# Kernel tuning notes

Hardware: AMD Instinct MI355X
Metric: run time of the kernel (lower is better)

The kernel has to match this reference:

```python
import jax, jax.numpy as jnp
import numpy as np

B, N, E, D, OUT, L = 4, 10000, 160000, 128, 64, 4
NEG = 0.01  # LeakyReLU slope

def lrelu(x):
    return jnp.where(x > 0, x, NEG * x)

def setup_inputs() -> dict:
    key = jax.random.key(0)
    ks = jax.random.split(key, 20)
    s = 0.05
    inp = {
        "x": jax.random.normal(ks[0], (B, N * 3), dtype=jnp.float32),
        "edge_index": jax.random.randint(ks[1], (2, E), 0, N, dtype=jnp.int32),
        # f0: Linear(3, D)
        "w0": jax.random.normal(ks[2], (3, D), dtype=jnp.float32) * s,
        "b0": jax.random.normal(ks[3], (D,), dtype=jnp.float32) * s,
        # per-layer params stacked on leading L axis
        "ew1": jax.random.normal(ks[4], (L, 2 * D + 1, D), dtype=jnp.float32) * s,
        "eb1": jax.random.normal(ks[5], (L, D), dtype=jnp.float32) * s,
        "ew2": jax.random.normal(ks[6], (L, D, D), dtype=jnp.float32) * s,
        "eb2": jax.random.normal(ks[7], (L, D), dtype=jnp.float32) * s,
        "cw": jax.random.normal(ks[8], (L, D, 1), dtype=jnp.float32) * s,
        "cb": jax.random.normal(ks[9], (L, 1), dtype=jnp.float32) * s,
        "nw1": jax.random.normal(ks[10], (L, 2 * D, D), dtype=jnp.float32) * s,
        "nb1": jax.random.normal(ks[11], (L, D), dtype=jnp.float32) * s,
        "nw2": jax.random.normal(ks[12], (L, D, D), dtype=jnp.float32) * s,
        "nb2": jax.random.normal(ks[13], (L, D), dtype=jnp.float32) * s,
        # project: Linear(D, OUT)
        "wp": jax.random.normal(ks[14], (D, OUT), dtype=jnp.float32) * s,
        "bp": jax.random.normal(ks[15], (OUT,), dtype=jnp.float32) * s,
    }
    return inp

def reference(x, edge_index, w0, b0, ew1, eb1, ew2, eb2, cw, cb, nw1, nb1, nw2, nb2, wp, bp):
    b = x.shape[0]
    n = x.shape[1] // 3
    pos = x.reshape(b, n, 3)            # coordinates [B,N,3]
    h = lrelu(pos @ w0 + b0)            # node features [B,N,D]
    row, col = edge_index[0], edge_index[1]
    # per-node in-edge counts (same for all layers/batches); scatter_mean -> 0 for empty nodes
    cnt = jnp.zeros((n,), x.dtype).at[col].add(1.0)
    denom = jnp.maximum(cnt, 1.0)[None, :, None]
    for i in range(L):
        rel = pos[:, row] - pos[:, col]                          # [B,E,3]
        dist_sq = jnp.sum(rel * rel, axis=-1, keepdims=True)     # [B,E,1]
        edge_in = jnp.concatenate([h[:, row], h[:, col], dist_sq], axis=-1)  # [B,E,2D+1]
        msg = lrelu(lrelu(edge_in @ ew1[i] + eb1[i]) @ ew2[i] + eb2[i])       # [B,E,D]
        aggr = jnp.zeros((b, n, msg.shape[-1]), msg.dtype).at[:, col].add(msg) / denom  # scatter_mean
        coord_update = jnp.tanh(aggr @ cw[i] + cb[i])            # [B,N,1]
        pos = pos + coord_update * 0.1
        node_in = jnp.concatenate([h, aggr], axis=-1)            # [B,N,2D]
        h = h + lrelu(lrelu(node_in @ nw1[i] + nb1[i]) @ nw2[i] + nb2[i])
    return lrelu(h.mean(axis=1) @ wp + bp)                       # [B,OUT]
```

## Files before the change

kernel.cpp:

```cpp
#include <hip/hip_runtime.h>
#include <hip/hip_bf16.h>
#include <math.h>

#define BB   4
#define NN   10000
#define NP   10112
#define EE   160000
#define DD   128
#define OUTD 64
#define LL   4
#define NEGS 0.01f
#define MSTR 136
#define RSF  34

typedef __attribute__((ext_vector_type(8))) short   short8;
typedef __attribute__((ext_vector_type(4))) float   floatx4;
typedef __attribute__((ext_vector_type(4))) uint    uintx4;

__device__ __forceinline__ float lrelu(float x) { return fmaxf(x, NEGS * x); }
__device__ __forceinline__ ushort f2bf(float x) {
    uint u = __builtin_bit_cast(uint, x);
    return (ushort)((u + 0x7FFFu + ((u >> 16) & 1u)) >> 16);
}
__device__ __forceinline__ float bf2f(ushort u) {
    uint v = ((uint)u) << 16;
    return __builtin_bit_cast(float, v);
}
__device__ __forceinline__ float bcf(uint u) { return __builtin_bit_cast(float, u); }

__global__ void k_cvtw_all(const float* __restrict__ ew1, const float* __restrict__ ew2,
                           const float* __restrict__ nw1, const float* __restrict__ nw2,
                           ushort* __restrict__ wtopf, ushort* __restrict__ wmidf,
                           ushort* __restrict__ ew2f, ushort* __restrict__ nw1f,
                           ushort* __restrict__ nw2f) {
    int tid = blockIdx.x * 256 + threadIdx.x;
    const float* src; ushort* dst; int pitch, nks, loc;
    if (tid < 8192)       { src = ew1;                     dst = wtopf; pitch = 257; nks = 4; loc = tid; }
    else if (tid < 16384) { src = ew1 + (size_t)128 * DD;  dst = wmidf; pitch = 257; nks = 4; loc = tid - 8192; }
    else if (tid < 24576) { src = ew2;                     dst = ew2f;  pitch = 128; nks = 4; loc = tid - 16384; }
    else if (tid < 40960) { src = nw1;                     dst = nw1f;  pitch = 256; nks = 8; loc = tid - 24576; }
    else                  { src = nw2;                     dst = nw2f;  pitch = 128; nks = 4; loc = tid - 40960; }
    int lane = loc & 63;
    int nt   = (loc >> 6) & 7;
    int ks   = (loc >> 9) % nks;
    int l    = loc / (nks * 512);
    int quad = lane >> 4, l16 = lane & 15;
    int n = nt * 16 + l16;
    const float* s = src + (size_t)l * pitch * DD;
    ushort* d = dst + (size_t)loc * 8;
    #pragma unroll
    for (int j = 0; j < 8; ++j)
        d[j] = f2bf(s[(size_t)(ks * 32 + quad * 8 + j) * DD + n]);
}

__global__ void k_h0(const float* __restrict__ x, const float* __restrict__ w0,
                     const float* __restrict__ b0, ushort* __restrict__ hb) {
    int idx = blockIdx.x * 256 + threadIdx.x;
    if (idx >= BB * NP * DD) return;
    int d  = idx & (DD - 1);
    int bn = idx >> 7;
    int n  = bn % NP, b = bn / NP;
    float v = 0.0f;
    if (n < NN) {
        const float* p = x + ((size_t)b * NN + n) * 3;
        v = lrelu(b0[d] + p[0] * w0[d] + p[1] * w0[DD + d] + p[2] * w0[2 * DD + d]);
    }
    hb[idx] = f2bf(v);
}

__global__ void k_count(const int* __restrict__ col, float* __restrict__ cnt,
                        int* __restrict__ ecnt) {
    int e = blockIdx.x * blockDim.x + threadIdx.x;
    if (e < EE) {
        int c = col[e];
        atomicAdd(&cnt[c], 1.0f);
        atomicAdd(&ecnt[c], 1);
    }
}

__global__ __launch_bounds__(256) void k_scan(const int* __restrict__ ecnt,
                                              int* __restrict__ cursor) {
    __shared__ int s_sum[256];
    int t = threadIdx.x;
    int base = t * 40;
    int s = 0;
    for (int i = 0; i < 40; ++i) {
        int n = base + i;
        if (n < NN) s += ecnt[n];
    }
    s_sum[t] = s;
    __syncthreads();
    if (t == 0) {
        int a = 0;
        for (int i = 0; i < 256; ++i) { int v = s_sum[i]; s_sum[i] = a; a += v; }
    }
    __syncthreads();
    int a = s_sum[t];
    for (int i = 0; i < 40; ++i) {
        int n = base + i;
        if (n < NN) { cursor[n] = a; a += ecnt[n]; }
    }
}

__global__ void k_place(const int* __restrict__ row, const int* __restrict__ col,
                        int* __restrict__ cursor,
                        int* __restrict__ rowS, int* __restrict__ colS) {
    int e = blockIdx.x * blockDim.x + threadIdx.x;
    if (e >= EE) return;
    int c = col[e];
    int p = atomicAdd(&cursor[c], 1);
    rowS[p] = row[e];
    colS[p] = c;
}

__global__ __launch_bounds__(256) void k_pq(
    const ushort* __restrict__ hb, const ushort* __restrict__ wtf,
    const ushort* __restrict__ wmf, const float* __restrict__ b1,
    ushort* __restrict__ P, ushort* __restrict__ Q)
{
    __shared__ __align__(16) ushort s_out[64 * MSTR];
    const int g = blockIdx.x;
    const int b = (g >> 1) & 3;
    const int n0 = ((g >> 3) * 2 + (g & 1)) * 64;
    const int t = threadIdx.x;
    const int w = t >> 6, lane = t & 63, quad = lane >> 4, l16 = lane & 15;
    const int rw = w * 16;
    const int nw = n0 + rw;

    const ushort* hptr = hb + ((size_t)b * NP + nw + l16) * DD;
    float b1r[8];
    #pragma unroll
    for (int nt = 0; nt < 8; ++nt) b1r[nt] = b1[nt * 16 + l16];

    const short8* wt = (const short8*)wtf;
    const short8* wm = (const short8*)wmf;

    #pragma unroll
    for (int pass = 0; pass < 2; ++pass) {
        floatx4 ap[8];
        #pragma unroll
        for (int nt = 0; nt < 8; ++nt)
            #pragma unroll
            for (int r = 0; r < 4; ++r) ap[nt][r] = pass ? b1r[nt] : 0.0f;
        const short8* wv = pass ? wm : wt;
        #pragma unroll
        for (int ks = 0; ks < 4; ++ks) {
            short8 bf[8];
            #pragma unroll
            for (int nt = 0; nt < 8; ++nt) bf[nt] = wv[(ks * 8 + nt) * 64 + lane];
            short8 af = *(const short8*)(hptr + ks * 32 + quad * 8);
            #pragma unroll
            for (int nt = 0; nt < 8; ++nt)
                ap[nt] = __builtin_amdgcn_mfma_f32_16x16x32_bf16(af, bf[nt], ap[nt], 0, 0, 0);
        }
        #pragma unroll
        for (int nt = 0; nt < 8; ++nt)
            #pragma unroll
            for (int r = 0; r < 4; ++r)
                s_out[(rw + quad * 4 + r) * MSTR + nt * 16 + l16] = f2bf(ap[nt][r]);
        ushort* dst = pass ? Q : P;
        #pragma unroll
        for (int i = 0; i < 4; ++i) {
            int row = rw + i * 4 + quad;
            short8 v = *(const short8*)&s_out[row * MSTR + l16 * 8];
            *(short8*)(dst + ((size_t)b * NP + n0 + row) * DD + l16 * 8) = v;
        }
    }
}

__global__ __launch_bounds__(256, 4) void k_edge(
    const float* __restrict__ pos,
    const ushort* __restrict__ P, const ushort* __restrict__ Q,
    const int* __restrict__ rowS, const int* __restrict__ colS,
    const float* __restrict__ w1last,
    const ushort* __restrict__ w2f, const float* __restrict__ b2,
    float* __restrict__ aggr)
{
    __shared__ __align__(16) int    s_col[128];
    __shared__ __align__(16) float  s_ds[128];
    __shared__ __align__(16) float  s_red[128 * RSF];
    __shared__ __align__(16) ushort s_w2[16384];
    __shared__ __align__(16) float  s_w1l[128];

    const int g    = blockIdx.x;
    const int b    = (g >> 1) & 3;
    const int tile = (g >> 3) * 2 + (g & 1);
    const int e0   = tile * 128;
    const int t    = threadIdx.x;
    const int w    = t >> 6, lane = t & 63;
    const int quad = lane >> 4, l16 = lane & 15;
    const int ew   = w * 32;

    const ushort* pp[2];
    const ushort* qp[2];
    #pragma unroll
    for (int mt = 0; mt < 2; ++mt) {
        int el = e0 + ew + mt * 16 + l16;
        pp[mt] = P + ((size_t)b * NP + rowS[el]) * DD;
        qp[mt] = Q + ((size_t)b * NP + colS[el]) * DD;
    }

    uintx4 pf[2][4], qf[2][4];
    #pragma unroll
    for (int ks = 0; ks < 4; ++ks) {
        const int koff = ks * 32 + quad * 8;
        #pragma unroll
        for (int mt = 0; mt < 2; ++mt) {
            pf[mt][ks] = *(const uintx4*)(pp[mt] + koff);
            qf[mt][ks] = *(const uintx4*)(qp[mt] + koff);
        }
    }

    if (t < 128) {
        int e = e0 + t;
        int r = rowS[e], c = colS[e];
        s_col[t] = c;
        const float* pr = pos + ((size_t)b * NN + r) * 3;
        const float* pc = pos + ((size_t)b * NN + c) * 3;
        float dx = pr[0] - pc[0], dy = pr[1] - pc[1], dz = pr[2] - pc[2];
        s_ds[t] = dx * dx + dy * dy + dz * dz;
    }
    {
        const short8* w2g = (const short8*)w2f;
        short8*       w2s = (short8*)s_w2;
        #pragma unroll
        for (int i = 0; i < 8; ++i)
            w2s[t + i * 256] = w2g[t + i * 256];
    }
    if (t < 32) ((floatx4*)s_w1l)[t] = ((const floatx4*)w1last)[t];
    __syncthreads();

    const int rh    = lane >> 5;
    const int colL  = lane & 31;
    const int rbase = ew + rh * 16;
    int bmask = 0, cid0;
    {
        int prev = s_col[rbase];
        cid0 = prev;
        #pragma unroll
        for (int r2 = 1; r2 < 16; ++r2) {
            int c = s_col[rbase + r2];
            if (c != prev) bmask |= (1 << r2);
            prev = c;
        }
    }

    float dsv[2];
    #pragma unroll
    for (int mt = 0; mt < 2; ++mt) dsv[mt] = s_ds[ew + mt * 16 + l16];

    uintx4 mid[2][4];
    #pragma unroll
    for (int ks = 0; ks < 4; ++ks) {
        const int koff = ks * 32 + quad * 8;
        floatx4 wl0 = *(const floatx4*)&s_w1l[koff];
        floatx4 wl1 = *(const floatx4*)&s_w1l[koff + 4];
        float wl[8] = {wl0[0], wl0[1], wl0[2], wl0[3], wl1[0], wl1[1], wl1[2], wl1[3]};
        #pragma unroll
        for (int mt = 0; mt < 2; ++mt) {
            #pragma unroll
            for (int i = 0; i < 4; ++i) {
                uint pv = pf[mt][ks][i], qv = qf[mt][ks][i];
                float vlo = lrelu(bcf(pv << 16) + bcf(qv << 16) + dsv[mt] * wl[2 * i]);
                float vhi = lrelu(bcf(pv & 0xFFFF0000u) + bcf(qv & 0xFFFF0000u) + dsv[mt] * wl[2 * i + 1]);
                mid[mt][ks][i] = __builtin_amdgcn_perm(
                    __builtin_bit_cast(uint, vhi), __builtin_bit_cast(uint, vlo), 0x07060302u);
            }
        }
    }

    float* aggr_bd = aggr + (size_t)b * NP * DD;

    const short8* w2s = (const short8*)s_w2;
    #pragma unroll
    for (int ph = 0; ph < 2; ++ph) {
        float b2r4[4];
        #pragma unroll
        for (int ntl = 0; ntl < 4; ++ntl) b2r4[ntl] = b2[(ph * 4 + ntl) * 16 + l16];

        floatx4 acc[2][4];
        #pragma unroll
        for (int mt = 0; mt < 2; ++mt)
            #pragma unroll
            for (int ntl = 0; ntl < 4; ++ntl)
                #pragma unroll
                for (int r = 0; r < 4; ++r) acc[mt][ntl][r] = b2r4[ntl];

        #pragma unroll
        for (int ks = 0; ks < 4; ++ks) {
            short8 bf[4];
            #pragma unroll
            for (int ntl = 0; ntl < 4; ++ntl)
                bf[ntl] = w2s[(ks * 8 + ph * 4 + ntl) * 64 + lane];
            #pragma unroll
            for (int mt = 0; mt < 2; ++mt) {
                short8 af = __builtin_bit_cast(short8, mid[mt][ks]);
                #pragma unroll
                for (int ntl = 0; ntl < 4; ++ntl)
                    acc[mt][ntl] = __builtin_amdgcn_mfma_f32_16x16x32_bf16(af, bf[ntl], acc[mt][ntl], 0, 0, 0);
            }
        }

        #pragma unroll
        for (int sp = 0; sp < 2; ++sp) {
            #pragma unroll
            for (int mt = 0; mt < 2; ++mt)
                #pragma unroll
                for (int j = 0; j < 2; ++j) {
                    const int ntl = sp * 2 + j;
                    #pragma unroll
                    for (int r = 0; r < 4; ++r)
                        s_red[(ew + mt * 16 + quad * 4 + r) * RSF + j * 16 + l16] =
                            lrelu(acc[mt][ntl][r]);
                }

            const int d = ph * 64 + sp * 32 + colL;
            float* ab = aggr_bd + d;
            float run = 0.0f;
            int cid = cid0;
            #pragma unroll
            for (int r = 0; r < 16; ++r) {
                float v = s_red[(rbase + r) * RSF + colL];
                if (bmask & (1 << r)) {
                    atomicAdd(ab + (size_t)cid * DD, run);
                    run = 0.0f;
                    cid = s_col[rbase + r];
                }
                run += v;
            }
            atomicAdd(ab + (size_t)cid * DD, run);
        }
    }
}

__global__ __launch_bounds__(256) void k_node(
    ushort* hb, float* aggr, const float* __restrict__ cnt,
    const float* __restrict__ cw, const float* __restrict__ cb,
    const ushort* __restrict__ w1f, const float* __restrict__ b1,
    const ushort* __restrict__ w2f, const float* __restrict__ b2,
    float* __restrict__ pos,
    int do_pq,
    const ushort* __restrict__ wtn, const ushort* __restrict__ wmn,
    const float* __restrict__ b1n,
    ushort* __restrict__ P, ushort* __restrict__ Q)
{
    __shared__ __align__(16) ushort s_mid[64 * MSTR];
    __shared__ __align__(16) ushort s_ho[64 * MSTR];

    const int g    = blockIdx.x;
    const int b    = (g >> 1) & 3;
    const int n0   = ((g >> 3) * 2 + (g & 1)) * 64;
    const int t    = threadIdx.x;
    const int w    = t >> 6, lane = t & 63;
    const int quad = lane >> 4, l16 = lane & 15;
    const int rw   = w * 16;
    const int nw   = n0 + rw;

    #pragma unroll
    for (int i = 0; i < 4; ++i) {
        int row = rw + i * 4 + quad;
        short8 v = *(const short8*)(hb + ((size_t)b * NP + n0 + row) * DD + l16 * 8);
        *(short8*)&s_ho[row * MSTR + l16 * 8] = v;
    }

    float* aptr = aggr + ((size_t)b * NP + nw + l16) * DD;
    float inv = 0.0f;
    {
        int node = nw + l16;
        if (node < NN) { float dn = cnt[node]; inv = 1.0f / fmaxf(dn, 1.0f); }
    }
    float b1r[8], b2r[8];
    #pragma unroll
    for (int nt = 0; nt < 8; ++nt) {
        int d = nt * 16 + l16;
        b1r[nt] = b1[d]; b2r[nt] = b2[d];
    }

    floatx4 acc[8];
    #pragma unroll
    for (int nt = 0; nt < 8; ++nt)
        #pragma unroll
        for (int r = 0; r < 4; ++r) acc[nt][r] = b1r[nt];

    float cwacc = 0.0f;
    const floatx4 zero4 = {0.0f, 0.0f, 0.0f, 0.0f};
    const short8* w1v = (const short8*)w1f;
    #pragma unroll
    for (int ks = 0; ks < 8; ++ks) {
        short8 bf[8];
        #pragma unroll
        for (int nt = 0; nt < 8; ++nt) bf[nt] = w1v[(ks * 8 + nt) * 64 + lane];
        const int koff = (ks & 3) * 32 + quad * 8;
        if (ks < 4) {
            short8 af = *(const short8*)(&s_ho[(rw + l16) * MSTR + koff]);
            #pragma unroll
            for (int nt = 0; nt < 8; ++nt)
                acc[nt] = __builtin_amdgcn_mfma_f32_16x16x32_bf16(af, bf[nt], acc[nt], 0, 0, 0);
        } else {
            floatx4 cw0 = *(const floatx4*)(cw + koff);
            floatx4 cw1 = *(const floatx4*)(cw + koff + 4);
            floatx4 a0 = *(const floatx4*)(aptr + koff);
            floatx4 a1 = *(const floatx4*)(aptr + koff + 4);
            *(floatx4*)(aptr + koff)     = zero4;
            *(floatx4*)(aptr + koff + 4) = zero4;
            short8 af;
            #pragma unroll
            for (int j = 0; j < 4; ++j) {
                float v = a0[j] * inv;
                af[j] = (short)f2bf(v);
                cwacc += v * cw0[j];
            }
            #pragma unroll
            for (int j = 0; j < 4; ++j) {
                float v = a1[j] * inv;
                af[4 + j] = (short)f2bf(v);
                cwacc += v * cw1[j];
            }
            #pragma unroll
            for (int nt = 0; nt < 8; ++nt)
                acc[nt] = __builtin_amdgcn_mfma_f32_16x16x32_bf16(af, bf[nt], acc[nt], 0, 0, 0);
        }
    }

    {
        float full = cwacc;
        full += __shfl_xor(full, 16);
        full += __shfl_xor(full, 32);
        int node = nw + l16;
        if (quad == 0 && node < NN) {
            float cu = 0.1f * tanhf(full + cb[0]);
            float* pp = pos + ((size_t)b * NN + node) * 3;
            pp[0] += cu; pp[1] += cu; pp[2] += cu;
        }
    }

    #pragma unroll
    for (int nt = 0; nt < 8; ++nt)
        #pragma unroll
        for (int r = 0; r < 4; ++r)
            s_mid[(rw + quad * 4 + r) * MSTR + nt * 16 + l16] = f2bf(lrelu(acc[nt][r]));

    floatx4 acc2[8];
    #pragma unroll
    for (int nt = 0; nt < 8; ++nt)
        #pragma unroll
        for (int r = 0; r < 4; ++r) acc2[nt][r] = b2r[nt];

    const short8* w2v = (const short8*)w2f;
    #pragma unroll
    for (int ks = 0; ks < 4; ++ks) {
        short8 bf[8];
        #pragma unroll
        for (int nt = 0; nt < 8; ++nt) bf[nt] = w2v[(ks * 8 + nt) * 64 + lane];
        short8 af = *(const short8*)(&s_mid[(rw + l16) * MSTR + ks * 32 + quad * 8]);
        #pragma unroll
        for (int nt = 0; nt < 8; ++nt)
            acc2[nt] = __builtin_amdgcn_mfma_f32_16x16x32_bf16(af, bf[nt], acc2[nt], 0, 0, 0);
    }

    #pragma unroll
    for (int nt = 0; nt < 8; ++nt)
        #pragma unroll
        for (int r = 0; r < 4; ++r) {
            int row = rw + quad * 4 + r;
            float hold = bf2f(s_ho[row * MSTR + nt * 16 + l16]);
            float hv = hold + lrelu(acc2[nt][r]);
            s_mid[row * MSTR + nt * 16 + l16] = f2bf(hv);
        }

    #pragma unroll
    for (int i = 0; i < 4; ++i) {
        int row = rw + i * 4 + quad;
        int n = n0 + row;
        short8 v = *(const short8*)&s_mid[row * MSTR + l16 * 8];
        if (n < NN)
            *(short8*)(hb + ((size_t)b * NP + n) * DD + l16 * 8) = v;
    }

    if (do_pq) {
        const short8* wt = (const short8*)wtn;
        const short8* wm = (const short8*)wmn;
        float b1nr[8];
        #pragma unroll
        for (int nt = 0; nt < 8; ++nt) b1nr[nt] = b1n[nt * 16 + l16];

        #pragma unroll
        for (int pass = 0; pass < 2; ++pass) {
            floatx4 ap[8];
            #pragma unroll
            for (int nt = 0; nt < 8; ++nt)
                #pragma unroll
                for (int r = 0; r < 4; ++r) ap[nt][r] = pass ? b1nr[nt] : 0.0f;
            const short8* wv = pass ? wm : wt;
            #pragma unroll
            for (int ks = 0; ks < 4; ++ks) {
                short8 bf[8];
                #pragma unroll
                for (int nt = 0; nt < 8; ++nt) bf[nt] = wv[(ks * 8 + nt) * 64 + lane];
                short8 af = *(const short8*)(&s_mid[(rw + l16) * MSTR + ks * 32 + quad * 8]);
                #pragma unroll
                for (int nt = 0; nt < 8; ++nt)
                    ap[nt] = __builtin_amdgcn_mfma_f32_16x16x32_bf16(af, bf[nt], ap[nt], 0, 0, 0);
            }
            #pragma unroll
            for (int nt = 0; nt < 8; ++nt)
                #pragma unroll
                for (int r = 0; r < 4; ++r)
                    s_ho[(rw + quad * 4 + r) * MSTR + nt * 16 + l16] = f2bf(ap[nt][r]);
            ushort* dst = pass ? Q : P;
            #pragma unroll
            for (int i = 0; i < 4; ++i) {
                int row = rw + i * 4 + quad;
                short8 v = *(const short8*)&s_ho[row * MSTR + l16 * 8];
                *(short8*)(dst + ((size_t)b * NP + n0 + row) * DD + l16 * 8) = v;
            }
        }
    }
}

#define NPC 50
__global__ void k_mean(const ushort* __restrict__ hb, float* __restrict__ hm) {
    int b  = blockIdx.y;
    int n0 = blockIdx.x * NPC;
    int d  = threadIdx.x;
    float s = 0.0f;
    for (int n = n0; n < n0 + NPC; ++n) s += bf2f(hb[((size_t)b * NP + n) * DD + d]);
    atomicAdd(&hm[b * DD + d], s);
}

__global__ void k_proj(const float* __restrict__ hm, const float* __restrict__ wp,
                       const float* __restrict__ bp, float* __restrict__ out) {
    int t = threadIdx.x;
    int b = t >> 6, o = t & (OUTD - 1);
    float s = 0.0f;
    for (int d2 = 0; d2 < DD; ++d2) s += hm[b * DD + d2] * wp[d2 * OUTD + o];
    s = s * (1.0f / NN) + bp[o];
    out[b * OUTD + o] = lrelu(s);
}

extern "C" void kernel_launch(void* const* d_in, const int* in_sizes, int n_in,
                              void* d_out, int out_size, void* d_ws, size_t ws_size,
                              hipStream_t stream) {
    (void)in_sizes; (void)n_in; (void)out_size; (void)ws_size;
    const float* x   = (const float*)d_in[0];
    const int*   ei  = (const int*)d_in[1];
    const float* w0  = (const float*)d_in[2];
    const float* b0  = (const float*)d_in[3];
    const float* ew1 = (const float*)d_in[4];
    const float* eb1 = (const float*)d_in[5];
    const float* ew2 = (const float*)d_in[6];
    const float* eb2 = (const float*)d_in[7];
    const float* cw  = (const float*)d_in[8];
    const float* cb  = (const float*)d_in[9];
    const float* nw1 = (const float*)d_in[10];
    const float* nb1 = (const float*)d_in[11];
    const float* nw2 = (const float*)d_in[12];
    const float* nb2 = (const float*)d_in[13];
    const float* wp  = (const float*)d_in[14];
    const float* bp  = (const float*)d_in[15];
    const int* row = ei;
    const int* col = ei + EE;

    const size_t HSZ = (size_t)BB * NP * DD;
    float* ws   = (float*)d_ws;
    float* aggr = ws;
    float* pos  = aggr + HSZ;
    float* cnt  = pos + (size_t)BB * NN * 3;
    float* hm   = cnt + NN;
    ushort* hb    = (ushort*)(hm + 512);
    ushort* Pb    = hb + HSZ;
    ushort* Qb    = Pb + HSZ;
    ushort* wtopf = Qb + HSZ;
    ushort* wmidf = wtopf + (size_t)LL * 16384;
    ushort* ew2f  = wmidf + (size_t)LL * 16384;
    ushort* nw1f  = ew2f + (size_t)LL * 16384;
    ushort* nw2f  = nw1f + (size_t)LL * 32768;
    int* ecnt   = (int*)(nw2f + (size_t)LL * 16384);
    int* cursor = ecnt + NN;
    int* rowS   = cursor + NN;
    int* colS   = rowS + EE;

    hipMemcpyAsync(pos, x, sizeof(float) * (size_t)BB * NN * 3,
                   hipMemcpyDeviceToDevice, stream);
    hipMemsetAsync(cnt, 0, sizeof(float) * NN, stream);
    hipMemsetAsync(ecnt, 0, sizeof(int) * NN, stream);
    hipMemsetAsync(hm, 0, sizeof(float) * BB * DD, stream);
    hipMemsetAsync(aggr, 0, sizeof(float) * HSZ, stream);

    k_cvtw_all<<<192, 256, 0, stream>>>(ew1, ew2, nw1, nw2,
                                        wtopf, wmidf, ew2f, nw1f, nw2f);

    k_h0<<<((int)HSZ + 255) / 256, 256, 0, stream>>>(x, w0, b0, hb);
    k_count<<<(EE + 255) / 256, 256, 0, stream>>>(col, cnt, ecnt);
    k_scan<<<1, 256, 0, stream>>>(ecnt, cursor);
    k_place<<<(EE + 255) / 256, 256, 0, stream>>>(row, col, cursor, rowS, colS);

    k_pq<<<(NP / 64) * BB, 256, 0, stream>>>(hb, wtopf, wmidf, eb1, Pb, Qb);

    for (int i = 0; i < LL; ++i) {
        k_edge<<<(EE / 128) * BB, 256, 0, stream>>>(
            pos, Pb, Qb, rowS, colS,
            ew1 + (size_t)i * 257 * DD + (size_t)256 * DD,
            ew2f + (size_t)i * 16384,
            eb2 + (size_t)i * DD,
            aggr);
        int nx = (i < LL - 1) ? (i + 1) : i;
        k_node<<<(NP / 64) * BB, 256, 0, stream>>>(
            hb, aggr, cnt,
            cw + (size_t)i * DD, cb + i,
            nw1f + (size_t)i * 32768, nb1 + (size_t)i * DD,
            nw2f + (size_t)i * 16384, nb2 + (size_t)i * DD,
            pos,
            (i < LL - 1) ? 1 : 0,
            wtopf + (size_t)nx * 16384, wmidf + (size_t)nx * 16384,
            eb1 + (size_t)nx * DD,
            Pb, Qb);
    }

    k_mean<<<dim3(NN / NPC, BB), DD, 0, stream>>>(hb, hm);
    k_proj<<<1, 256, 0, stream>>>(hm, wp, bp, (float*)d_out);
}
```

Before: 590.0 us.

## Make edge kernel persistent over several edge tiles to amortize W2 staging

The edge kernel now handles five consecutive 128-edge tiles per block in a loop instead of one, so the 32KB W2 weight copy into shared memory and the bias loads happen once per five tiles. The grid shrinks by five, and the batch index moves to the low bits of the block index. The cost is less parallelism (1000 → 1000/... blocks total 1000), an extra barrier per tile, and no overlap of the gather loads with the previous tile's compute inside a block.

After: 609.4 us. +3.3%, slower.

```diff
diff --git a/kernel.cpp b/kernel.cpp
--- a/kernel.cpp
+++ b/kernel.cpp
@@ -12,6 +12,7 @@
 #define NEGS 0.01f
 #define MSTR 136
 #define RSF  34
+#define TPB  5
 
 typedef __attribute__((ext_vector_type(8))) short   short8;
 typedef __attribute__((ext_vector_type(4))) float   floatx4;
@@ -183,43 +184,21 @@
     __shared__ __align__(16) float  s_w1l[128];
 
     const int g    = blockIdx.x;
-    const int b    = (g >> 1) & 3;
-    const int tile = (g >> 3) * 2 + (g & 1);
-    const int e0   = tile * 128;
+    const int b    = g & 3;
+    const int t0   = (g >> 2) * TPB;
     const int t    = threadIdx.x;
     const int w    = t >> 6, lane = t & 63;
     const int quad = lane >> 4, l16 = lane & 15;
     const int ew   = w * 32;
-
-    const ushort* pp[2];
-    const ushort* qp[2];
-    #pragma unroll
-    for (int mt = 0; mt < 2; ++mt) {
-        int el = e0 + ew + mt * 16 + l16;
-        pp[mt] = P + ((size_t)b * NP + rowS[el]) * DD;
-        qp[mt] = Q + ((size_t)b * NP + colS[el]) * DD;
-    }
-
-    uintx4 pf[2][4], qf[2][4];
-    #pragma unroll
-    for (int ks = 0; ks < 4; ++ks) {
-        const int koff = ks * 32 + quad * 8;
-        #pragma unroll
-        for (int mt = 0; mt < 2; ++mt) {
-            pf[mt][ks] = *(const uintx4*)(pp[mt] + koff);
-            qf[mt][ks] = *(const uintx4*)(qp[mt] + koff);
-        }
-    }
-
-    if (t < 128) {
-        int e = e0 + t;
-        int r = rowS[e], c = colS[e];
-        s_col[t] = c;
-        const float* pr = pos + ((size_t)b * NN + r) * 3;
-        const float* pc = pos + ((size_t)b * NN + c) * 3;
-        float dx = pr[0] - pc[0], dy = pr[1] - pc[1], dz = pr[2] - pc[2];
-        s_ds[t] = dx * dx + dy * dy + dz * dz;
-    }
+    const int rh    = lane >> 5;
+    const int colL  = lane & 31;
+    const int rbase = ew + rh * 16;
+
+    const ushort* Pb_  = P + (size_t)b * NP * DD;
+    const ushort* Qb_  = Q + (size_t)b * NP * DD;
+    const float*  posb = pos + (size_t)b * NN * 3;
+    float* aggr_bd = aggr + (size_t)b * NP * DD;
+
     {
         const short8* w2g = (const short8*)w2f;
         short8*       w2s = (short8*)s_w2;
@@ -228,108 +207,137 @@
             w2s[t + i * 256] = w2g[t + i * 256];
     }
     if (t < 32) ((floatx4*)s_w1l)[t] = ((const floatx4*)w1last)[t];
-    __syncthreads();
-
-    const int rh    = lane >> 5;
-    const int colL  = lane & 31;
-    const int rbase = ew + rh * 16;
-    int bmask = 0, cid0;
-    {
-        int prev = s_col[rbase];
-        cid0 = prev;
-        #pragma unroll
-        for (int r2 = 1; r2 < 16; ++r2) {
-            int c = s_col[rbase + r2];
-            if (c != prev) bmask |= (1 << r2);
-            prev = c;
-        }
-    }
-
-    float dsv[2];
-    #pragma unroll
-    for (int mt = 0; mt < 2; ++mt) dsv[mt] = s_ds[ew + mt * 16 + l16];
-
-    uintx4 mid[2][4];
-    #pragma unroll
-    for (int ks = 0; ks < 4; ++ks) {
-        const int koff = ks * 32 + quad * 8;
-        floatx4 wl0 = *(const floatx4*)&s_w1l[koff];
-        floatx4 wl1 = *(const floatx4*)&s_w1l[koff + 4];
-        float wl[8] = {wl0[0], wl0[1], wl0[2], wl0[3], wl1[0], wl1[1], wl1[2], wl1[3]};
+    float b2r[8];
+    #pragma unroll
+    for (int nt = 0; nt < 8; ++nt) b2r[nt] = b2[nt * 16 + l16];
+
+    const short8* w2s = (const short8*)s_w2;
+
+    #pragma unroll 1
+    for (int it = 0; it < TPB; ++it) {
+        const int e0 = (t0 + it) * 128;
+
+        const ushort* pp[2];
+        const ushort* qp[2];
         #pragma unroll
         for (int mt = 0; mt < 2; ++mt) {
-            #pragma unroll
-            for (int i = 0; i < 4; ++i) {
-                uint pv = pf[mt][ks][i], qv = qf[mt][ks][i];
-                float vlo = lrelu(bcf(pv << 16) + bcf(qv << 16) + dsv[mt] * wl[2 * i]);
-                float vhi = lrelu(bcf(pv & 0xFFFF0000u) + bcf(qv & 0xFFFF0000u) + dsv[mt] * wl[2 * i + 1]);
-                mid[mt][ks][i] = __builtin_amdgcn_perm(
-                    __builtin_bit_cast(uint, vhi), __builtin_bit_cast(uint, vlo), 0x07060302u);
-            }
-        }
-    }
-
-    float* aggr_bd = aggr + (size_t)b * NP * DD;
-
-    const short8* w2s = (const short8*)s_w2;
-    #pragma unroll
-    for (int ph = 0; ph < 2; ++ph) {
-        float b2r4[4];
-        #pragma unroll
-        for (int ntl = 0; ntl < 4; ++ntl) b2r4[ntl] = b2[(ph * 4 + ntl) * 16 + l16];
-
-        floatx4 acc[2][4];
-        #pragma unroll
-        for (int mt = 0; mt < 2; ++mt)
-            #pragma unroll
-            for (int ntl = 0; ntl < 4; ++ntl)
-                #pragma unroll
-                for (int r = 0; r < 4; ++r) acc[mt][ntl][r] = b2r4[ntl];
-
+            int el = e0 + ew + mt * 16 + l16;
+            pp[mt] = Pb_ + (size_t)rowS[el] * DD;
+            qp[mt] = Qb_ + (size_t)colS[el] * DD;
+        }
+        uintx4 pf[2][4], qf[2][4];
         #pragma unroll
         for (int ks = 0; ks < 4; ++ks) {
-            short8 bf[4];
-            #pragma unroll
-            for (int ntl = 0; ntl < 4; ++ntl)
-                bf[ntl] = w2s[(ks * 8 + ph * 4 + ntl) * 64 + lane];
+            const int koff = ks * 32 + quad * 8;
             #pragma unroll
             for (int mt = 0; mt < 2; ++mt) {
-                short8 af = __builtin_bit_cast(short8, mid[mt][ks]);
+                pf[mt][ks] = *(const uintx4*)(pp[mt] + koff);
+                qf[mt][ks] = *(const uintx4*)(qp[mt] + koff);
+            }
+        }
+
+        if (t < 128) {
+            int e = e0 + t;
+            int r = rowS[e], c = colS[e];
+            s_col[t] = c;
+            const float* pr = posb + (size_t)r * 3;
+            const float* pc = posb + (size_t)c * 3;
+            float dx = pr[0] - pc[0], dy = pr[1] - pc[1], dz = pr[2] - pc[2];
+            s_ds[t] = dx * dx + dy * dy + dz * dz;
+        }
+        __syncthreads();
+
+        int bmask = 0, cid0;
+        {
+            int prev = s_col[rbase];
+            cid0 = prev;
+            #pragma unroll
+            for (int r2 = 1; r2 < 16; ++r2) {
+                int c = s_col[rbase + r2];
+                if (c != prev) bmask |= (1 << r2);
+                prev = c;
+            }
+        }
+        float dsv[2];
+        #pragma unroll
+        for (int mt = 0; mt < 2; ++mt) dsv[mt] = s_ds[ew + mt * 16 + l16];
+
+        uintx4 mid[2][4];
+        #pragma unroll
+        for (int ks = 0; ks < 4; ++ks) {
+            const int koff = ks * 32 + quad * 8;
+            floatx4 wl0 = *(const floatx4*)&s_w1l[koff];
+            floatx4 wl1 = *(const floatx4*)&s_w1l[koff + 4];
+            float wl[8] = {wl0[0], wl0[1], wl0[2], wl0[3], wl1[0], wl1[1], wl1[2], wl1[3]};
+            #pragma unroll
+            for (int mt = 0; mt < 2; ++mt) {
+                #pragma unroll
+                for (int i = 0; i < 4; ++i) {
+                    uint pv = pf[mt][ks][i], qv = qf[mt][ks][i];
+                    float vlo = lrelu(bcf(pv << 16) + bcf(qv << 16) + dsv[mt] * wl[2 * i]);
+                    float vhi = lrelu(bcf(pv & 0xFFFF0000u) + bcf(qv & 0xFFFF0000u) + dsv[mt] * wl[2 * i + 1]);
+                    mid[mt][ks][i] = __builtin_amdgcn_perm(
+                        __builtin_bit_cast(uint, vhi), __builtin_bit_cast(uint, vlo), 0x07060302u);
+                }
+            }
+        }
+
+        #pragma unroll
+        for (int ph = 0; ph < 2; ++ph) {
+            floatx4 acc[2][4];
+            #pragma unroll
+            for (int mt = 0; mt < 2; ++mt)
                 #pragma unroll
                 for (int ntl = 0; ntl < 4; ++ntl)
-                    acc[mt][ntl] = __builtin_amdgcn_mfma_f32_16x16x32_bf16(af, bf[ntl], acc[mt][ntl], 0, 0, 0);
-            }
-        }
-
-        #pragma unroll
-        for (int sp = 0; sp < 2; ++sp) {
-            #pragma unroll
-            for (int mt = 0; mt < 2; ++mt)
-                #pragma unroll
-                for (int j = 0; j < 2; ++j) {
-                    const int ntl = sp * 2 + j;
                     #pragma unroll
-                    for (int r = 0; r < 4; ++r)
-                        s_red[(ew + mt * 16 + quad * 4 + r) * RSF + j * 16 + l16] =
-                            lrelu(acc[mt][ntl][r]);
+                    for (int r = 0; r < 4; ++r) acc[mt][ntl][r] = b2r[ph * 4 + ntl];
+
+            #pragma unroll
+            for (int ks = 0; ks < 4; ++ks) {
+                short8 bf[4];
+                #pragma unroll
+                for (int ntl = 0; ntl < 4; ++ntl)
+                    bf[ntl] = w2s[(ks * 8 + ph * 4 + ntl) * 64 + lane];
+                #pragma unroll
+                for (int mt = 0; mt < 2; ++mt) {
+                    short8 af = __builtin_bit_cast(short8, mid[mt][ks]);
+                    #pragma unroll
+                    for (int ntl = 0; ntl < 4; ++ntl)
+                        acc[mt][ntl] = __builtin_amdgcn_mfma_f32_16x16x32_bf16(af, bf[ntl], acc[mt][ntl], 0, 0, 0);
                 }
-
-            const int d = ph * 64 + sp * 32 + colL;
-            float* ab = aggr_bd + d;
-            float run = 0.0f;
-            int cid = cid0;
-            #pragma unroll
-            for (int r = 0; r < 16; ++r) {
-                float v = s_red[(rbase + r) * RSF + colL];
-                if (bmask & (1 << r)) {
-                    atomicAdd(ab + (size_t)cid * DD, run);
-                    run = 0.0f;
-                    cid = s_col[rbase + r];
+            }
+
+            #pragma unroll
+            for (int sp = 0; sp < 2; ++sp) {
+                #pragma unroll
+                for (int mt = 0; mt < 2; ++mt)
+                    #pragma unroll
+                    for (int j = 0; j < 2; ++j) {
+                        const int ntl = sp * 2 + j;
+                        #pragma unroll
+                        for (int r = 0; r < 4; ++r)
+                            s_red[(ew + mt * 16 + quad * 4 + r) * RSF + j * 16 + l16] =
+                                lrelu(acc[mt][ntl][r]);
+                    }
+
+                const int d = ph * 64 + sp * 32 + colL;
+                float* ab = aggr_bd + d;
+                float run = 0.0f;
+                int cid = cid0;
+                #pragma unroll
+                for (int r = 0; r < 16; ++r) {
+                    float v = s_red[(rbase + r) * RSF + colL];
+                    if (bmask & (1 << r)) {
+                        atomicAdd(ab + (size_t)cid * DD, run);
+                        run = 0.0f;
+                        cid = s_col[rbase + r];
+                    }
+                    run += v;
                 }
-                run += v;
-            }
-            atomicAdd(ab + (size_t)cid * DD, run);
-        }
+                atomicAdd(ab + (size_t)cid * DD, run);
+            }
+        }
+        __syncthreads();
     }
 }
 
@@ -598,7 +606,7 @@
     k_pq<<<(NP / 64) * BB, 256, 0, stream>>>(hb, wtopf, wmidf, eb1, Pb, Qb);
 
     for (int i = 0; i < LL; ++i) {
-        k_edge<<<(EE / 128) * BB, 256, 0, stream>>>(
+        k_edge<<<(EE / 128 / TPB) * BB, 256, 0, stream>>>(
             pos, Pb, Qb, rowS, colS,
             ew1 + (size_t)i * 257 * DD + (size_t)256 * DD,
             ew2f + (size_t)i * 16384,
```
